# Kernel optimization log

Hardware: AMD Instinct MI355X
Metric: run time of the kernel (lower is better)

The kernel has to match this reference:

```python
import jax, jax.numpy as jnp
import numpy as np

B, S, E, H = 2, 2048, 1024, 16
HD = E // H


def setup_inputs() -> dict:
    key = jax.random.key(0)
    ks = jax.random.split(key, 5)
    scale = 0.02
    return {
        "x": jax.random.normal(ks[0], (B, S, E), dtype=jnp.float32),
        "qkv_w": jax.random.normal(ks[1], (3 * E, E), dtype=jnp.float32) * scale,
        "qkv_b": jax.random.normal(ks[2], (3 * E,), dtype=jnp.float32) * scale,
        "out_w": jax.random.normal(ks[3], (E, E), dtype=jnp.float32) * scale,
        "out_b": jax.random.normal(ks[4], (E,), dtype=jnp.float32) * scale,
    }


def reference(x, qkv_w, qkv_b, out_w, out_b):
    b, s, e = x.shape
    scale = 1.0 / jnp.sqrt(jnp.float32(HD))
    # fused QKV projection: torch Linear is x @ W.T + b
    qkv = x @ qkv_w.T + qkv_b                       # [b, s, 3e]
    qkv = qkv.reshape(b, s, 3, H, HD)
    qkv = jnp.transpose(qkv, (2, 0, 3, 1, 4))       # [3, b, h, s, hd]
    q, k, v = qkv[0], qkv[1], qkv[2]
    scores = jnp.einsum('bhqd,bhkd->bhqk', q, k) * scale
    # causal mask (atmask=True): mask strictly upper triangle
    causal = jnp.triu(jnp.ones((s, s), dtype=bool), k=1)
    scores = jnp.where(causal, -jnp.inf, scores)
    attn = jax.nn.softmax(scores, axis=-1)          # dropout p=0.0 -> identity
    out = jnp.einsum('bhqk,bhkd->bhqd', attn, v)    # [b, h, s, hd]
    out = jnp.transpose(out, (0, 2, 1, 3)).reshape(b, s, e)
    return out @ out_w.T + out_b
```

## Files before the change

kernel.cpp:

```cpp
#include <hip/hip_runtime.h>
#include <cmath>

typedef __attribute__((ext_vector_type(8))) __bf16 bf16x8;
typedef __attribute__((ext_vector_type(8))) unsigned short ushort8v;
typedef __attribute__((ext_vector_type(4))) float f32x4;

__device__ inline unsigned short f2bf(float f) {
    unsigned int u = __float_as_uint(f);
    unsigned int r = (u + 0x7fffu + ((u >> 16) & 1u)) >> 16;
    return (unsigned short)r;
}

__device__ inline bf16x8 ld8(const unsigned short* p) {
    uint4 v = *(const uint4*)p;
    return __builtin_bit_cast(bf16x8, v);
}

__device__ inline f32x4 mfma16(bf16x8 a, bf16x8 b, f32x4 c) {
    return __builtin_amdgcn_mfma_f32_16x16x32_bf16(a, b, c, 0, 0, 0);
}

__device__ inline unsigned pk2t(float a, float b) {
    return __builtin_amdgcn_perm(__float_as_uint(b), __float_as_uint(a), 0x07060302u);
}

__device__ inline void gl_lds16(const unsigned short* g, const unsigned short* l) {
    __builtin_amdgcn_global_load_lds(
        (const __attribute__((address_space(1))) void*)(unsigned long long)g,
        (__attribute__((address_space(3))) void*)(unsigned)(unsigned long long)l,
        16, 0, 0);
}

#define NX4  1048576
#define NW14 786432
#define NW24 262144
__global__ __launch_bounds__(256) void cvt3(const float* __restrict__ x,
                                            const float* __restrict__ w1,
                                            const float* __restrict__ w2,
                                            unsigned short* __restrict__ xb,
                                            unsigned short* __restrict__ w1b,
                                            unsigned short* __restrict__ w2b) {
    int i = blockIdx.x * 256 + threadIdx.x;
    const float* src;
    unsigned short* dst;
    int off;
    if (i < NX4)              { src = x;  dst = xb;  off = i; }
    else if (i < NX4 + NW14)  { src = w1; dst = w1b; off = i - NX4; }
    else                      { src = w2; dst = w2b; off = i - NX4 - NW14; }
    float4 v = ((const float4*)src)[off];
    ushort4 o;
    o.x = f2bf(v.x); o.y = f2bf(v.y); o.z = f2bf(v.z); o.w = f2bf(v.w);
    ((ushort4*)dst)[off] = o;
}

__global__ __launch_bounds__(256) void gemm_out(const unsigned short* __restrict__ A,
                                                const unsigned short* __restrict__ B,
                                                const float* __restrict__ bias,
                                                float* __restrict__ C,
                                                int M, int N, int K) {
    __shared__ __align__(16) unsigned short As0[64 * 32];
    __shared__ __align__(16) unsigned short Bs0[128 * 32];
    __shared__ __align__(16) unsigned short As1[64 * 32];
    __shared__ __align__(16) unsigned short Bs1[128 * 32];
    const int m0 = blockIdx.y * 64;
    const int n0 = blockIdx.x * 128;
    const int t = threadIdx.x;
    const int wave = t >> 6, lane = t & 63;
    const int l16 = lane & 15, quad = lane >> 4;
    const int wm = (wave >> 1) * 32, wn = (wave & 1) * 64;

    f32x4 acc[2][4] = {};

    const int ra = t >> 2, ka = (t & 3) * 8;
    const int b1 = 256 + t;
    const int rb0 = t >> 2, kb0 = (t & 3) * 8;
    const int rb1 = b1 >> 2, kb1 = (b1 & 3) * 8;

    for (int k0 = 0; k0 < K; k0 += 64) {
        __syncthreads();
        gl_lds16(A + (size_t)(m0 + ra) * K + k0 + ka,        As0 + t * 8);
        gl_lds16(B + (size_t)(n0 + rb0) * K + k0 + kb0,      Bs0 + t * 8);
        gl_lds16(B + (size_t)(n0 + rb1) * K + k0 + kb1,      Bs0 + b1 * 8);
        gl_lds16(A + (size_t)(m0 + ra) * K + k0 + 32 + ka,   As1 + t * 8);
        gl_lds16(B + (size_t)(n0 + rb0) * K + k0 + 32 + kb0, Bs1 + t * 8);
        gl_lds16(B + (size_t)(n0 + rb1) * K + k0 + 32 + kb1, Bs1 + b1 * 8);
        __syncthreads();

        bf16x8 af[2], bfr[4];
        #pragma unroll
        for (int i = 0; i < 2; ++i)
            af[i] = ld8(As0 + (wm + i * 16 + l16) * 32 + quad * 8);
        #pragma unroll
        for (int j = 0; j < 4; ++j)
            bfr[j] = ld8(Bs0 + (wn + j * 16 + l16) * 32 + quad * 8);
        #pragma unroll
        for (int i = 0; i < 2; ++i)
            #pragma unroll
            for (int j = 0; j < 4; ++j)
                acc[i][j] = mfma16(af[i], bfr[j], acc[i][j]);

        #pragma unroll
        for (int i = 0; i < 2; ++i)
            af[i] = ld8(As1 + (wm + i * 16 + l16) * 32 + quad * 8);
        #pragma unroll
        for (int j = 0; j < 4; ++j)
            bfr[j] = ld8(Bs1 + (wn + j * 16 + l16) * 32 + quad * 8);
        #pragma unroll
        for (int i = 0; i < 2; ++i)
            #pragma unroll
            for (int j = 0; j < 4; ++j)
                acc[i][j] = mfma16(af[i], bfr[j], acc[i][j]);
    }

    #pragma unroll
    for (int i = 0; i < 2; ++i) {
        #pragma unroll
        for (int j = 0; j < 4; ++j) {
            int col = n0 + wn + j * 16 + l16;
            float bv = bias[col];
            #pragma unroll
            for (int r = 0; r < 4; ++r) {
                int row = m0 + wm + i * 16 + quad * 4 + r;
                C[(size_t)row * N + col] = acc[i][j][r] + bv;
            }
        }
    }
}

__global__ __launch_bounds__(256) void gemm_qkv(const unsigned short* __restrict__ A,
                                                const unsigned short* __restrict__ B,
                                                const float* __restrict__ bias,
                                                unsigned short* __restrict__ qp,
                                                unsigned short* __restrict__ kvp,
                                                int M, int N, int K) {
    __shared__ __align__(16) unsigned short Ep[12288];
    unsigned short* As0 = Ep;
    unsigned short* As1 = Ep + 2048;
    unsigned short* Bs0 = Ep + 4096;
    unsigned short* Bs1 = Ep + 8192;
    const int m0 = blockIdx.y * 64;
    const int n0 = blockIdx.x * 128;
    const int t = threadIdx.x;
    const int wave = t >> 6, lane = t & 63;
    const int l16 = lane & 15, quad = lane >> 4;
    const int wm = (wave >> 1) * 32, wn = (wave & 1) * 64;

    f32x4 acc[2][4] = {};

    const int ra = t >> 2, ka = (t & 3) * 8;
    const int b1 = 256 + t;
    const int rb0 = t >> 2, kb0 = (t & 3) * 8;
    const int rb1 = b1 >> 2, kb1 = (b1 & 3) * 8;

    for (int k0 = 0; k0 < K; k0 += 64) {
        __syncthreads();
        gl_lds16(A + (size_t)(m0 + ra) * K + k0 + ka,        As0 + t * 8);
        gl_lds16(B + (size_t)(n0 + rb0) * K + k0 + kb0,      Bs0 + t * 8);
        gl_lds16(B + (size_t)(n0 + rb1) * K + k0 + kb1,      Bs0 + b1 * 8);
        gl_lds16(A + (size_t)(m0 + ra) * K + k0 + 32 + ka,   As1 + t * 8);
        gl_lds16(B + (size_t)(n0 + rb0) * K + k0 + 32 + kb0, Bs1 + t * 8);
        gl_lds16(B + (size_t)(n0 + rb1) * K + k0 + 32 + kb1, Bs1 + b1 * 8);
        __syncthreads();

        bf16x8 af[2], bfr[4];
        #pragma unroll
        for (int i = 0; i < 2; ++i)
            af[i] = ld8(As0 + (wm + i * 16 + l16) * 32 + quad * 8);
        #pragma unroll
        for (int j = 0; j < 4; ++j)
            bfr[j] = ld8(Bs0 + (wn + j * 16 + l16) * 32 + quad * 8);
        #pragma unroll
        for (int i = 0; i < 2; ++i)
            #pragma unroll
            for (int j = 0; j < 4; ++j)
                acc[i][j] = mfma16(af[i], bfr[j], acc[i][j]);

        #pragma unroll
        for (int i = 0; i < 2; ++i)
            af[i] = ld8(As1 + (wm + i * 16 + l16) * 32 + quad * 8);
        #pragma unroll
        for (int j = 0; j < 4; ++j)
            bfr[j] = ld8(Bs1 + (wn + j * 16 + l16) * 32 + quad * 8);
        #pragma unroll
        for (int i = 0; i < 2; ++i)
            #pragma unroll
            for (int j = 0; j < 4; ++j)
                acc[i][j] = mfma16(af[i], bfr[j], acc[i][j]);
    }

    __syncthreads();
    const int b = m0 >> 11;

    if (n0 < 1024) {
        #pragma unroll
        for (int j = 0; j < 4; ++j) {
            int cl = wn + j * 16 + l16;
            float bv = bias[n0 + cl];
            int hrel = cl >> 6, d = cl & 63;
            int half = d >> 5, qd = d & 31;
            int obase = hrel * 4096 + half * 512 + (qd >> 3) * 128 + quad * 32 + (qd & 7);
            #pragma unroll
            for (int i = 0; i < 2; ++i) {
                int ob = obase + ((wm + i * 16) >> 4) * 1024;
                #pragma unroll
                for (int r = 0; r < 4; ++r)
                    Ep[ob + r * 8] = f2bf((acc[i][j][r] + bv) * 0.180336880f);
            }
        }
        __syncthreads();
        const int h0 = n0 >> 6, qt0 = (m0 & 2047) >> 4;
        #pragma unroll
        for (int k = 0; k < 4; ++k) {
            int u = t + 256 * k;
            int cq = u >> 7, within = u & 127;
            int bh = b * 16 + h0 + (cq >> 2);
            int qt = qt0 + (cq & 3);
            *(uint4*)(qp + (size_t)(bh * 128 + qt) * 1024 + within * 8) =
                *(const uint4*)(Ep + u * 8);
        }
    } else if (n0 < 2048) {
        const int f2 = (quad & 1) * 2, qh = 4 * (quad >> 1);
        #pragma unroll
        for (int j = 0; j < 4; ++j) {
            int cl = wn + j * 16 + l16;
            float bv = bias[n0 + cl];
            int hrel = cl >> 6, d = cl & 63;
            int fbit0 = d >> 5, qd = d & 31;
            int obase = hrel * 4096 + (wm >> 5) * 2048 + (f2 | fbit0) * 512 +
                        (qd >> 3) * 128 + qh * 8 + (qd & 7);
            #pragma unroll
            for (int i = 0; i < 2; ++i) {
                int ob = obase + i * 64;
                #pragma unroll
                for (int r = 0; r < 4; ++r)
                    Ep[ob + r * 8] = f2bf(acc[i][j][r] + bv);
            }
        }
        __syncthreads();
        const int h0 = (n0 - 1024) >> 6, tile0 = (m0 & 2047) >> 5;
        #pragma unroll
        for (int k = 0; k < 4; ++k) {
            int u = t + 256 * k;
            int ck = u >> 8, within = u & 255;
            int bh = b * 16 + h0 + (ck >> 1);
            int tile = tile0 + (ck & 1);
            *(uint4*)(kvp + (size_t)(bh * 64 + tile) * 4096 + within * 8) =
                *(const uint4*)(Ep + u * 8);
        }
    } else {
        const int kr = quad >> 1, e4 = (quad & 1) * 4;
        #pragma unroll
        for (int j = 0; j < 4; ++j) {
            int cl = wn + j * 16 + l16;
            float bv = bias[n0 + cl];
            int hrel = cl >> 6, d = cl & 63;
            int tn = d >> 4, l16v = d & 15;
            int obase = hrel * 4096 + (wm >> 5) * 2048 + tn * 512 +
                        (kr * 16 + l16v) * 8 + e4;
            #pragma unroll
            for (int i = 0; i < 2; ++i) {
                int ob = obase + i * 256;
                unsigned short tmp[4];
                #pragma unroll
                for (int r = 0; r < 4; ++r) tmp[r] = f2bf(acc[i][j][r] + bv);
                *(unsigned long long*)(Ep + ob) = *(const unsigned long long*)tmp;
            }
        }
        __syncthreads();
        const int h0 = (n0 - 2048) >> 6, tile0 = (m0 & 2047) >> 5;
        #pragma unroll
        for (int k = 0; k < 4; ++k) {
            int u = t + 256 * k;
            int ck = u >> 8, within = u & 255;
            int bh = b * 16 + h0 + (ck >> 1);
            int tile = tile0 + (ck & 1);
            *(uint4*)(kvp + (size_t)(bh * 64 + tile) * 4096 + 2048 + within * 8) =
                *(const uint4*)(Ep + u * 8);
        }
    }
}

__global__ __launch_bounds__(256, 2) void attn_kernel(const unsigned short* __restrict__ qp,
                                                      const unsigned short* __restrict__ kvp,
                                                      unsigned short* __restrict__ out) {
    const int S = 2048, E = 1024;
    const int wavei = threadIdx.x >> 6;
    const int lane = threadIdx.x & 63;
    const int l16 = lane & 15, quad = lane >> 4;
    const int bidx = blockIdx.x;
    const int bh = (bidx & 7) * 4 + ((bidx >> 3) & 3);
    const int P = 31 - (bidx >> 5);
    const int b = bh >> 4, h = bh & 15;
    const int loff = lane * 8;

    const unsigned short* qbase = qp + (size_t)(bh * 128 + 4 * P) * 1024;
    bf16x8 bq[4][2];
    #pragma unroll
    for (int g = 0; g < 4; ++g) {
        bq[g][0] = ld8(qbase + (2 * g) * 512 + loff);
        bq[g][1] = ld8(qbase + (2 * g + 1) * 512 + loff);
    }

    ushort8v ov;
    #pragma unroll
    for (int j = 0; j < 8; ++j) ov[j] = 0x3F80;
    const bf16x8 ones = __builtin_bit_cast(bf16x8, ov);

    f32x4 O[4][4] = {};
    f32x4 L[4] = {};
    const int nchunks = P + 1;
    const unsigned short* tbase = kvp + (size_t)bh * 64 * 4096;

    for (int c = wavei; c < nchunks; c += 4) {
        const unsigned short* tb = tbase + (size_t)c * 8192;
        bf16x8 f[16];
        #pragma unroll
        for (int i = 0; i < 16; ++i) f[i] = ld8(tb + i * 512 + loff);

        const bool lastc = (c == nchunks - 1);
        const int ks = c * 64;

        #pragma unroll
        for (int tile = 0; tile < 2; ++tile) {
            const bf16x8* g8 = f + tile * 8;
            const int kst = ks + tile * 32;

            f32x4 s0[4], s1[4];
            #pragma unroll
            for (int g = 0; g < 4; ++g) { s0[g] = {}; s1[g] = {}; }
            #pragma unroll
            for (int g = 0; g < 4; ++g) {
                s0[g] = mfma16(g8[0], bq[g][0], s0[g]);
                s0[g] = mfma16(g8[1], bq[g][1], s0[g]);
                s1[g] = mfma16(g8[2], bq[g][0], s1[g]);
                s1[g] = mfma16(g8[3], bq[g][1], s1[g]);
            }

            bf16x8 bp[4];
            #pragma unroll
            for (int g = 0; g < 4; ++g) {
                float p0[4], p1[4];
                if (lastc) {
                    const int qg = 64 * P + 16 * g + l16;
                    #pragma unroll
                    for (int r = 0; r < 4; ++r) {
                        int kk = kst + quad * 8 + r;
                        p0[r] = (kk > qg)     ? 0.f : __builtin_amdgcn_exp2f(s0[g][r]);
                        p1[r] = (kk + 4 > qg) ? 0.f : __builtin_amdgcn_exp2f(s1[g][r]);
                    }
                } else {
                    #pragma unroll
                    for (int r = 0; r < 4; ++r) {
                        p0[r] = __builtin_amdgcn_exp2f(s0[g][r]);
                        p1[r] = __builtin_amdgcn_exp2f(s1[g][r]);
                    }
                }
                uint4 pw;
                pw.x = pk2t(p0[0], p0[1]);
                pw.y = pk2t(p0[2], p0[3]);
                pw.z = pk2t(p1[0], p1[1]);
                pw.w = pk2t(p1[2], p1[3]);
                bp[g] = __builtin_bit_cast(bf16x8, pw);
            }

            #pragma unroll
            for (int g = 0; g < 4; ++g) {
                O[g][0] = mfma16(g8[4], bp[g], O[g][0]);
                O[g][1] = mfma16(g8[5], bp[g], O[g][1]);
                O[g][2] = mfma16(g8[6], bp[g], O[g][2]);
                O[g][3] = mfma16(g8[7], bp[g], O[g][3]);
                L[g]    = mfma16(ones, bp[g], L[g]);
            }
        }
    }

    __shared__ float Ob[4][64][66];
    __shared__ float Lb[4][64];
    #pragma unroll
    for (int g = 0; g < 4; ++g) {
        #pragma unroll
        for (int tn = 0; tn < 4; ++tn)
            #pragma unroll
            for (int r = 0; r < 4; ++r)
                Ob[wavei][g * 16 + l16][tn * 16 + quad * 4 + r] = O[g][tn][r];
        if (quad == 0) Lb[wavei][g * 16 + l16] = L[g][0];
    }
    __syncthreads();

    const int t = threadIdx.x;
    const int qi = t >> 2, hg = (t & 3) * 16;
    float ls = Lb[0][qi] + Lb[1][qi] + Lb[2][qi] + Lb[3][qi];
    const float invl = 1.0f / ls;
    const size_t obase = (size_t)(b * S + 64 * P + qi) * E + h * 64;
    #pragma unroll
    for (int part = 0; part < 2; ++part) {
        int hd0 = hg + part * 8;
        unsigned short o[8];
        #pragma unroll
        for (int k = 0; k < 8; ++k) {
            float a = Ob[0][qi][hd0 + k] + Ob[1][qi][hd0 + k] +
                      Ob[2][qi][hd0 + k] + Ob[3][qi][hd0 + k];
            o[k] = f2bf(a * invl);
        }
        *(uint4*)(out + obase + hd0) = *(uint4*)o;
    }
}

extern "C" void kernel_launch(void* const* d_in, const int* in_sizes, int n_in,
                              void* d_out, int out_size, void* d_ws, size_t ws_size,
                              hipStream_t stream) {
    const float* x     = (const float*)d_in[0];
    const float* qkv_w = (const float*)d_in[1];
    const float* qkv_b = (const float*)d_in[2];
    const float* out_w = (const float*)d_in[3];
    const float* out_b = (const float*)d_in[4];
    float* out = (float*)d_out;

    const int B = 2, S = 2048, E = 1024;
    const int M = B * S;
    const int N1 = 3 * E;

    unsigned short* ws    = (unsigned short*)d_ws;
    unsigned short* xb    = ws;
    unsigned short* w1b   = xb   + (size_t)M * E;
    unsigned short* w2b   = w1b  + (size_t)N1 * E;
    unsigned short* qpb   = w2b  + (size_t)E * E;
    unsigned short* kvpb  = qpb  + (size_t)32 * 128 * 1024;
    unsigned short* attnb = kvpb + (size_t)32 * 64 * 4096;

    cvt3<<<dim3(8192), dim3(256), 0, stream>>>(x, qkv_w, out_w, xb, w1b, w2b);

    gemm_qkv<<<dim3(N1 / 128, M / 64), dim3(256), 0, stream>>>(
        xb, w1b, qkv_b, qpb, kvpb, M, N1, E);

    attn_kernel<<<dim3(1024), dim3(256), 0, stream>>>(qpb, kvpb, attnb);

    gemm_out<<<dim3(E / 128, M / 64), dim3(256), 0, stream>>>(
        attnb, w2b, out_b, out, M, E, E);
}
```

Baseline: 165.4 us.

## Double-buffer K/V register fragments and raise wave priority around MFMA blocks

Restructures the attention chunk loop into a software pipeline with two register buffers. The next chunk's K/V fragments load while the current chunk computes, so global-load latency is meant to hide behind MFMA work. It also wraps the MFMA groups in s_setprio to favour matrix issue across waves. The extra 16 bf16x8 registers per lane raise register pressure and may reduce occupancy or cause spills.

```diff
diff --git a/kernel.cpp b/kernel.cpp
--- a/kernel.cpp
+++ b/kernel.cpp
@@ -311,68 +311,94 @@
     const int nchunks = P + 1;
     const unsigned short* tbase = kvp + (size_t)bh * 64 * 4096;
 
-    for (int c = wavei; c < nchunks; c += 4) {
-        const unsigned short* tb = tbase + (size_t)c * 8192;
-        bf16x8 f[16];
-        #pragma unroll
-        for (int i = 0; i < 16; ++i) f[i] = ld8(tb + i * 512 + loff);
-
-        const bool lastc = (c == nchunks - 1);
-        const int ks = c * 64;
-
-        #pragma unroll
-        for (int tile = 0; tile < 2; ++tile) {
-            const bf16x8* g8 = f + tile * 8;
-            const int kst = ks + tile * 32;
-
-            f32x4 s0[4], s1[4];
-            #pragma unroll
-            for (int g = 0; g < 4; ++g) { s0[g] = {}; s1[g] = {}; }
-            #pragma unroll
-            for (int g = 0; g < 4; ++g) {
-                s0[g] = mfma16(g8[0], bq[g][0], s0[g]);
-                s0[g] = mfma16(g8[1], bq[g][1], s0[g]);
-                s1[g] = mfma16(g8[2], bq[g][0], s1[g]);
-                s1[g] = mfma16(g8[3], bq[g][1], s1[g]);
+#define LOADF(F, C) do { \
+    const unsigned short* tb_ = tbase + (size_t)(C) * 8192; \
+    _Pragma("unroll") \
+    for (int i_ = 0; i_ < 16; ++i_) (F)[i_] = ld8(tb_ + i_ * 512 + loff); \
+} while (0)
+
+#define COMPUTE(F, C) do { \
+    const bool lastc_ = ((C) == nchunks - 1); \
+    const int ks_ = (C) * 64; \
+    _Pragma("unroll") \
+    for (int tile = 0; tile < 2; ++tile) { \
+        const bf16x8* g8 = (F) + tile * 8; \
+        const int kst = ks_ + tile * 32; \
+        f32x4 s0[4], s1[4]; \
+        _Pragma("unroll") \
+        for (int g = 0; g < 4; ++g) { s0[g] = {}; s1[g] = {}; } \
+        __builtin_amdgcn_s_setprio(1); \
+        _Pragma("unroll") \
+        for (int g = 0; g < 4; ++g) { \
+            s0[g] = mfma16(g8[0], bq[g][0], s0[g]); \
+            s0[g] = mfma16(g8[1], bq[g][1], s0[g]); \
+            s1[g] = mfma16(g8[2], bq[g][0], s1[g]); \
+            s1[g] = mfma16(g8[3], bq[g][1], s1[g]); \
+        } \
+        __builtin_amdgcn_s_setprio(0); \
+        bf16x8 bp[4]; \
+        _Pragma("unroll") \
+        for (int g = 0; g < 4; ++g) { \
+            float p0[4], p1[4]; \
+            if (lastc_) { \
+                const int qg = 64 * P + 16 * g + l16; \
+                _Pragma("unroll") \
+                for (int r = 0; r < 4; ++r) { \
+                    int kk = kst + quad * 8 + r; \
+                    p0[r] = (kk > qg)     ? 0.f : __builtin_amdgcn_exp2f(s0[g][r]); \
+                    p1[r] = (kk + 4 > qg) ? 0.f : __builtin_amdgcn_exp2f(s1[g][r]); \
+                } \
+            } else { \
+                _Pragma("unroll") \
+                for (int r = 0; r < 4; ++r) { \
+                    p0[r] = __builtin_amdgcn_exp2f(s0[g][r]); \
+                    p1[r] = __builtin_amdgcn_exp2f(s1[g][r]); \
+                } \
+            } \
+            uint4 pw; \
+            pw.x = pk2t(p0[0], p0[1]); \
+            pw.y = pk2t(p0[2], p0[3]); \
+            pw.z = pk2t(p1[0], p1[1]); \
+            pw.w = pk2t(p1[2], p1[3]); \
+            bp[g] = __builtin_bit_cast(bf16x8, pw); \
+        } \
+        __builtin_amdgcn_s_setprio(1); \
+        _Pragma("unroll") \
+        for (int g = 0; g < 4; ++g) { \
+            O[g][0] = mfma16(g8[4], bp[g], O[g][0]); \
+            O[g][1] = mfma16(g8[5], bp[g], O[g][1]); \
+            O[g][2] = mfma16(g8[6], bp[g], O[g][2]); \
+            O[g][3] = mfma16(g8[7], bp[g], O[g][3]); \
+            L[g]    = mfma16(ones, bp[g], L[g]); \
+        } \
+        __builtin_amdgcn_s_setprio(0); \
+    } \
+} while (0)
+
+    {
+        int c = wavei;
+        if (c < nchunks) {
+            bf16x8 fA[16], fB[16];
+            LOADF(fA, c);
+            while (c + 4 < nchunks) {
+                LOADF(fB, c + 4);
+                COMPUTE(fA, c);
+                c += 4;
+                if (c + 4 < nchunks) {
+                    LOADF(fA, c + 4);
+                    COMPUTE(fB, c);
+                    c += 4;
+                } else {
+                    COMPUTE(fB, c);
+                    goto merged;
+                }
             }
-
-            bf16x8 bp[4];
-            #pragma unroll
-            for (int g = 0; g < 4; ++g) {
-                float p0[4], p1[4];
-                if (lastc) {
-                    const int qg = 64 * P + 16 * g + l16;
-                    #pragma unroll
-                    for (int r = 0; r < 4; ++r) {
-                        int kk = kst + quad * 8 + r;
-                        p0[r] = (kk > qg)     ? 0.f : __builtin_amdgcn_exp2f(s0[g][r]);
-                        p1[r] = (kk + 4 > qg) ? 0.f : __builtin_amdgcn_exp2f(s1[g][r]);
-                    }
-                } else {
-                    #pragma unroll
-                    for (int r = 0; r < 4; ++r) {
-                        p0[r] = __builtin_amdgcn_exp2f(s0[g][r]);
-                        p1[r] = __builtin_amdgcn_exp2f(s1[g][r]);
-                    }
-                }
-                uint4 pw;
-                pw.x = pk2t(p0[0], p0[1]);
-                pw.y = pk2t(p0[2], p0[3]);
-                pw.z = pk2t(p1[0], p1[1]);
-                pw.w = pk2t(p1[2], p1[3]);
-                bp[g] = __builtin_bit_cast(bf16x8, pw);
-            }
-
-            #pragma unroll
-            for (int g = 0; g < 4; ++g) {
-                O[g][0] = mfma16(g8[4], bp[g], O[g][0]);
-                O[g][1] = mfma16(g8[5], bp[g], O[g][1]);
-                O[g][2] = mfma16(g8[6], bp[g], O[g][2]);
-                O[g][3] = mfma16(g8[7], bp[g], O[g][3]);
-                L[g]    = mfma16(ones, bp[g], L[g]);
-            }
-        }
-    }
+            COMPUTE(fA, c);
+            merged:;
+        }
+    }
+#undef LOADF
+#undef COMPUTE
 
     __shared__ float Ob[4][64][66];
     __shared__ float Lb[4][64];
```

Result: slower. 254.1 us (+53.6%).
